# Optimization experiments

Hardware: AMD Instinct MI355X
Metric: run time of the kernel (lower is better)

The kernel has to match this reference:

```python
import jax, jax.numpy as jnp
import numpy as np

B, S, D, F, E = 4, 2048, 1024, 4096, 8


def setup_inputs() -> dict:
    key = jax.random.key(0)
    ks = jax.random.split(key, 7)
    s1 = 1.0 / np.sqrt(D)
    s2 = 1.0 / np.sqrt(F)
    x = jax.random.normal(ks[0], (B, S, D), dtype=jnp.float32)
    # Stacked expert weights: linear1 (D->F), linear2 (F->D), torch default uniform init
    W1 = jax.random.uniform(ks[1], (E, D, F), jnp.float32, -s1, s1)
    b1 = jax.random.uniform(ks[2], (E, F), jnp.float32, -s1, s1)
    W2 = jax.random.uniform(ks[3], (E, F, D), jnp.float32, -s2, s2)
    b2 = jax.random.uniform(ks[4], (E, D), jnp.float32, -s2, s2)
    Wr = jax.random.uniform(ks[5], (D, E), jnp.float32, -s1, s1)
    br = jax.random.uniform(ks[6], (E,), jnp.float32, -s1, s1)
    return {"x": x, "W1": W1, "b1": b1, "W2": W2, "b2": b2, "Wr": Wr, "br": br}


def reference(x, W1, b1, W2, b2, Wr, br):
    b, s, d = x.shape
    e = Wr.shape[1]
    logits = x @ Wr + br                      # [B,S,E]
    idx = jnp.argmax(logits, axis=-1)         # top-1 expert per token
    probs = jax.nn.softmax(logits, axis=-1)
    gates = jnp.take_along_axis(probs, idx[..., None], axis=-1)[..., 0]  # [B,S]
    xf = x.reshape(-1, d)                     # [N,D]
    idxf = idx.reshape(-1)
    gf = gates.reshape(-1)
    out = jnp.zeros_like(xf)
    for ei in range(e):                       # fixed small expert count
        h = jax.nn.gelu(xf @ W1[ei] + b1[ei], approximate=False)  # exact gelu like F.gelu
        y = h @ W2[ei] + b2[ei]
        mask = (idxf == ei).astype(xf.dtype)
        out = out + y * (gf * mask)[:, None]
    return out.reshape(b, s, d)
```

## Files before the change

### kernel.cpp

```cpp
#include <hip/hip_runtime.h>
#include <stdint.h>
#include <math.h>

#define NTOK 8192
#define DIM  1024
#define FDIM 4096
#define NEXP 8

typedef __bf16 bf16x8 __attribute__((ext_vector_type(8)));
typedef float floatx4 __attribute__((ext_vector_type(4)));
typedef unsigned int u32;

__device__ __forceinline__ unsigned short f2b(float f) {
  union { float f; unsigned u; } v; v.f = f;
  return (unsigned short)((v.u + 0x7fffu + ((v.u >> 16) & 1u)) >> 16);
}

__device__ __forceinline__ float gelu_f(float x) {
  float u = 1.5957691216f * x * (1.0f + 0.044715f * x * x);
  return x / (1.0f + __expf(-u));
}

__device__ __forceinline__ void async_cp16(const unsigned short* g, unsigned short* l) {
  __builtin_amdgcn_global_load_lds((__attribute__((address_space(1))) u32*)g,
                                   (__attribute__((address_space(3))) u32*)l, 16, 0, 0);
}

__device__ __forceinline__ void expert_tile(const int* __restrict__ ctrl, int mt,
                                            int& e, int& m0, int& cnt, int& ntiles) {
  int off = 0, ts = 0;
  e = 0; m0 = 0; cnt = 0;
#pragma unroll
  for (int i = 0; i < NEXP; i++) {
    int c = ctrl[i];
    int nt = (c + 127) >> 7;
    if (mt >= ts && mt < ts + nt) {
      e = i;
      m0 = off + (mt - ts) * 128;
      cnt = c - (mt - ts) * 128;
    }
    ts += nt; off += c;
  }
  ntiles = ts;
  if (cnt > 128) cnt = 128;
}

__global__ __launch_bounds__(256) void router_k(
    const float* __restrict__ x, const float* __restrict__ Wr,
    const float* __restrict__ br, int* __restrict__ idx,
    float* __restrict__ gate, int* __restrict__ ctrl) {
  int t = (int)((blockIdx.x * 256 + threadIdx.x) >> 6);
  int lane = threadIdx.x & 63;
  const float* xr = x + (size_t)t * DIM;
  float acc[NEXP];
#pragma unroll
  for (int e = 0; e < NEXP; e++) acc[e] = 0.f;
#pragma unroll
  for (int k = 0; k < DIM / 64; k++) {
    int d = k * 64 + lane;
    float xv = xr[d];
    const float4* wp = (const float4*)(Wr + (size_t)d * NEXP);
    float4 w0 = wp[0], w1 = wp[1];
    acc[0] += xv * w0.x; acc[1] += xv * w0.y;
    acc[2] += xv * w0.z; acc[3] += xv * w0.w;
    acc[4] += xv * w1.x; acc[5] += xv * w1.y;
    acc[6] += xv * w1.z; acc[7] += xv * w1.w;
  }
#pragma unroll
  for (int off = 32; off > 0; off >>= 1) {
#pragma unroll
    for (int e = 0; e < NEXP; e++) acc[e] += __shfl_xor(acc[e], off, 64);
  }
  if (lane == 0) {
    float mx = -3.4e38f; int best = 0;
#pragma unroll
    for (int e = 0; e < NEXP; e++) {
      float l = acc[e] + br[e];
      if (l > mx) { mx = l; best = e; }
    }
    float s = 0.f;
#pragma unroll
    for (int e = 0; e < NEXP; e++) s += expf(acc[e] + br[e] - mx);
    idx[t] = best;
    gate[t] = 1.f / s;
    atomicAdd(&ctrl[best], 1);
  }
}

__global__ __launch_bounds__(256) void scatter_k(
    const float* __restrict__ x, const int* __restrict__ idx,
    const float* __restrict__ gate, int* __restrict__ ctrl,
    unsigned short* __restrict__ Xb, int* __restrict__ token_dst,
    float* __restrict__ gate_p) {
  __shared__ int s_pos;
  int t = blockIdx.x;
  if (threadIdx.x == 0) {
    int e = idx[t];
    int off = 0;
#pragma unroll
    for (int i = 0; i < NEXP; i++) off += (i < e) ? ctrl[i] : 0;
    s_pos = off + atomicAdd(&ctrl[17 + e], 1);
  }
  __syncthreads();
  int pos = s_pos;
  if (threadIdx.x == 0) { token_dst[pos] = t; gate_p[pos] = gate[t]; }
  float4 v = ((const float4*)(x + (size_t)t * DIM))[threadIdx.x];
  ushort4 o;
  o.x = f2b(v.x); o.y = f2b(v.y); o.z = f2b(v.z); o.w = f2b(v.w);
  ((ushort4*)(Xb + (size_t)pos * DIM))[threadIdx.x] = o;
}

__global__ __launch_bounds__(256) void transpose_cvt2_k(
    const float* __restrict__ W1, unsigned short* __restrict__ W1b,
    const float* __restrict__ W2, unsigned short* __restrict__ W2b) {
  __shared__ float tile[64][65];
  __shared__ unsigned short obuf[64][72];
  int z = blockIdx.z;
  const float* in; unsigned short* out; int R, C, tc, tr;
  if (z < NEXP) {
    in = W1 + (size_t)z * DIM * FDIM; out = W1b + (size_t)z * DIM * FDIM;
    R = DIM; C = FDIM; tc = blockIdx.x; tr = blockIdx.y;
  } else {
    int e = z - NEXP;
    in = W2 + (size_t)e * FDIM * DIM; out = W2b + (size_t)e * FDIM * DIM;
    R = FDIM; C = DIM; tc = blockIdx.y; tr = blockIdx.x;
  }
  int c0 = tc * 64, r0 = tr * 64;
  int t = threadIdx.x;
  int rr = t >> 4, cc = (t & 15) * 4;
#pragma unroll
  for (int k = 0; k < 64; k += 16) {
    float4 v = *(const float4*)&in[(size_t)(r0 + rr + k) * C + c0 + cc];
    tile[rr + k][cc] = v.x; tile[rr + k][cc + 1] = v.y;
    tile[rr + k][cc + 2] = v.z; tile[rr + k][cc + 3] = v.w;
  }
  __syncthreads();
  int cr = t >> 4, rb = (t & 15) * 4;
#pragma unroll
  for (int k = 0; k < 64; k += 16) {
    ushort4 o;
    o.x = f2b(tile[rb + 0][cr + k]); o.y = f2b(tile[rb + 1][cr + k]);
    o.z = f2b(tile[rb + 2][cr + k]); o.w = f2b(tile[rb + 3][cr + k]);
    *(ushort4*)&obuf[cr + k][rb] = o;
  }
  __syncthreads();
  int r2 = t >> 3, c8 = (t & 7) * 8;
#pragma unroll
  for (int k = 0; k < 64; k += 32)
    *(uint4*)&out[(size_t)(c0 + r2 + k) * R + r0 + c8] = *(const uint4*)&obuf[r2 + k][c8];
}

__global__ __launch_bounds__(256) void gemm1_k(
    const unsigned short* __restrict__ Amat, const unsigned short* __restrict__ Bmat,
    const float* __restrict__ bias, unsigned short* __restrict__ Hout,
    const int* __restrict__ ctrl) {
  __shared__ unsigned short lds[17408];
  unsigned short* A_lds = lds;
  unsigned short* B_lds = lds + 8192;

  int mt = blockIdx.y;
  int e, m0, cnt, ntiles;
  expert_tile(ctrl, mt, e, m0, cnt, ntiles);
  if (mt >= ntiles) return;
  int c0 = blockIdx.x * 128;
  const unsigned short* B = Bmat + (size_t)e * FDIM * DIM;

  int tid = threadIdx.x;
  int lane = tid & 63, wave = tid >> 6;
  int wr = wave >> 1, wc = wave & 1;
  int grp = lane >> 4, m16 = lane & 15;

  int lr = lane >> 3;
  int cchunk = (lane & 7) ^ lr;
  const unsigned short* srcA[4];
  const unsigned short* srcB[4];
  unsigned short* dstA[4];
  unsigned short* dstB[4];
#pragma unroll
  for (int q = 0; q < 4; q++) {
    int brow = wave * 32 + q * 8;
    int arow = m0 + brow + lr; if (arow > NTOK - 1) arow = NTOK - 1;
    srcA[q] = Amat + (size_t)arow * DIM + cchunk * 8;
    srcB[q] = B + (size_t)(c0 + brow + lr) * DIM + cchunk * 8;
    dstA[q] = A_lds + brow * 64;
    dstB[q] = B_lds + brow * 64;
  }

  floatx4 acc[4][4];
  floatx4 zero = {0.f, 0.f, 0.f, 0.f};
#pragma unroll
  for (int i = 0; i < 4; i++)
#pragma unroll
    for (int j = 0; j < 4; j++) acc[i][j] = zero;

  int x7 = m16 & 7;
  int rowA[4], rowB[4];
#pragma unroll
  for (int i = 0; i < 4; i++) {
    rowA[i] = (wr * 64 + i * 16 + m16) * 64;
    rowB[i] = (wc * 64 + i * 16 + m16) * 64;
  }

  for (int kk = 0; kk < DIM; kk += 64) {
#pragma unroll
    for (int q = 0; q < 4; q++) async_cp16(srcA[q], dstA[q]);
#pragma unroll
    for (int q = 0; q < 4; q++) async_cp16(srcB[q], dstB[q]);
#pragma unroll
    for (int q = 0; q < 4; q++) { srcA[q] += 64; srcB[q] += 64; }
    __syncthreads();
    bf16x8 af[2][4], bfr[2][4];
#pragma unroll
    for (int h = 0; h < 2; h++) {
      int off = (((h << 2) | grp) ^ x7) << 3;
#pragma unroll
      for (int i = 0; i < 4; i++) {
        af[h][i]  = *(const bf16x8*)&A_lds[rowA[i] + off];
        bfr[h][i] = *(const bf16x8*)&B_lds[rowB[i] + off];
      }
    }
#pragma unroll
    for (int h = 0; h < 2; h++)
#pragma unroll
      for (int i = 0; i < 4; i++)
#pragma unroll
        for (int j = 0; j < 4; j++)
          acc[i][j] = __builtin_amdgcn_mfma_f32_16x16x32_bf16(af[h][i], bfr[h][j], acc[i][j], 0, 0, 0);
    __syncthreads();
  }

  float bs[4];
#pragma unroll
  for (int j = 0; j < 4; j++) bs[j] = bias[(size_t)e * FDIM + c0 + wc * 64 + j * 16 + m16];

  unsigned short* st = lds + wave * 4352;
#pragma unroll
  for (int i = 0; i < 4; i++)
#pragma unroll
    for (int j = 0; j < 4; j++)
#pragma unroll
      for (int r = 0; r < 4; r++)
        st[(i * 16 + grp * 4 + r) * 68 + j * 16 + m16] = f2b(gelu_f(acc[i][j][r] + bs[j]));
  __syncthreads();
  int lr8 = lane >> 3, c8 = (lane & 7) * 8;
  int colb = c0 + wc * 64 + c8;
#pragma unroll
  for (int rr = 0; rr < 8; rr++) {
    int row = rr * 8 + lr8;
    int gm = wr * 64 + row;
    if (gm < cnt) {
      uint2 a = *(const uint2*)&st[row * 68 + c8];
      uint2 b = *(const uint2*)&st[row * 68 + c8 + 4];
      uint4 v; v.x = a.x; v.y = a.y; v.z = b.x; v.w = b.y;
      *(uint4*)&Hout[(size_t)(m0 + gm) * FDIM + colb] = v;
    }
  }
}

__global__ __launch_bounds__(256) void gemm2_k(
    const unsigned short* __restrict__ Hmat, const unsigned short* __restrict__ W2b,
    const float* __restrict__ b2, float* __restrict__ out,
    const int* __restrict__ token_dst, const float* __restrict__ gate_p,
    const int* __restrict__ ctrl) {
  __shared__ unsigned short lds[32768];

  int mt = blockIdx.y;
  int e, m0, cnt, ntiles;
  expert_tile(ctrl, mt, e, m0, cnt, ntiles);
  if (mt >= ntiles) return;
  int c0 = blockIdx.x * 128;
  const unsigned short* B = W2b + (size_t)e * DIM * FDIM;

  int tid = threadIdx.x;
  int lane = tid & 63, wave = tid >> 6;
  int wr = wave >> 1, wc = wave & 1;
  int grp = lane >> 4, m16 = lane & 15;

  int lr = lane >> 3;
  int cchunk = (lane & 7) ^ lr;
  const unsigned short* srcA[4];
  const unsigned short* srcB[4];
  int dstoff[4];
#pragma unroll
  for (int q = 0; q < 4; q++) {
    int brow = wave * 32 + q * 8;
    int arow = m0 + brow + lr; if (arow > NTOK - 1) arow = NTOK - 1;
    srcA[q] = Hmat + (size_t)arow * FDIM + cchunk * 8;
    srcB[q] = B + (size_t)(c0 + brow + lr) * FDIM + cchunk * 8;
    dstoff[q] = brow * 64;
  }

  floatx4 acc[4][4];
  floatx4 zero = {0.f, 0.f, 0.f, 0.f};
#pragma unroll
  for (int i = 0; i < 4; i++)
#pragma unroll
    for (int j = 0; j < 4; j++) acc[i][j] = zero;

  int x7 = m16 & 7;
  int rowA[4], rowB[4];
#pragma unroll
  for (int i = 0; i < 4; i++) {
    rowA[i] = (wr * 64 + i * 16 + m16) * 64;
    rowB[i] = (wc * 64 + i * 16 + m16) * 64;
  }

#pragma unroll
  for (int q = 0; q < 4; q++) async_cp16(srcA[q], lds + dstoff[q]);
#pragma unroll
  for (int q = 0; q < 4; q++) async_cp16(srcB[q], lds + 8192 + dstoff[q]);
#pragma unroll
  for (int q = 0; q < 4; q++) { srcA[q] += 64; srcB[q] += 64; }

  const int kIters = FDIM / 64;
  int p = 0;
  for (int it = 0; it < kIters; ++it) {
    __syncthreads();
    unsigned short* Acur = lds + p * 16384;
    unsigned short* Bcur = Acur + 8192;
    if (it + 1 < kIters) {
      unsigned short* An = lds + (p ^ 1) * 16384;
      unsigned short* Bn = An + 8192;
#pragma unroll
      for (int q = 0; q < 4; q++) async_cp16(srcA[q], An + dstoff[q]);
#pragma unroll
      for (int q = 0; q < 4; q++) async_cp16(srcB[q], Bn + dstoff[q]);
#pragma unroll
      for (int q = 0; q < 4; q++) { srcA[q] += 64; srcB[q] += 64; }
    }
    bf16x8 af[2][4], bfr[2][4];
#pragma unroll
    for (int h = 0; h < 2; h++) {
      int off = (((h << 2) | grp) ^ x7) << 3;
#pragma unroll
      for (int i = 0; i < 4; i++) {
        af[h][i]  = *(const bf16x8*)&Acur[rowA[i] + off];
        bfr[h][i] = *(const bf16x8*)&Bcur[rowB[i] + off];
      }
    }
#pragma unroll
    for (int h = 0; h < 2; h++)
#pragma unroll
      for (int i = 0; i < 4; i++)
#pragma unroll
        for (int j = 0; j < 4; j++)
          acc[i][j] = __builtin_amdgcn_mfma_f32_16x16x32_bf16(af[h][i], bfr[h][j], acc[i][j], 0, 0, 0);
    p ^= 1;
  }

  float bs[4];
#pragma unroll
  for (int j = 0; j < 4; j++) bs[j] = b2[(size_t)e * DIM + c0 + wc * 64 + j * 16 + m16];

#pragma unroll
  for (int i = 0; i < 4; i++) {
    int rb = wr * 64 + i * 16 + grp * 4;
#pragma unroll
    for (int r = 0; r < 4; r++) {
      int lm = rb + r;
      if (lm < cnt) {
        int t = token_dst[m0 + lm];
        float g = gate_p[m0 + lm];
#pragma unroll
        for (int j = 0; j < 4; j++) {
          int col = c0 + wc * 64 + j * 16 + m16;
          out[(size_t)t * DIM + col] = (acc[i][j][r] + bs[j]) * g;
        }
      }
    }
  }
}

extern "C" void kernel_launch(void* const* d_in, const int* in_sizes, int n_in,
                              void* d_out, int out_size, void* d_ws, size_t ws_size,
                              hipStream_t stream) {
  const float* x  = (const float*)d_in[0];
  const float* W1 = (const float*)d_in[1];
  const float* b1 = (const float*)d_in[2];
  const float* W2 = (const float*)d_in[3];
  const float* b2 = (const float*)d_in[4];
  const float* Wr = (const float*)d_in[5];
  const float* br = (const float*)d_in[6];
  float* out = (float*)d_out;

  char* w = (char*)d_ws;
  int*   ctrl      = (int*)w;
  int*   idx       = (int*)(w + 1024);
  float* gate      = (float*)(w + 1024 + 4 * NTOK);
  int*   token_dst = (int*)(w + 1024 + 8 * NTOK);
  float* gate_p    = (float*)(w + 1024 + 12 * NTOK);
  unsigned short* Xb  = (unsigned short*)(w + (1ull << 18));
  unsigned short* H   = (unsigned short*)(w + (20ull << 20));
  unsigned short* W1b = (unsigned short*)(w + (88ull << 20));
  unsigned short* W2b = (unsigned short*)(w + (156ull << 20));

  hipMemsetAsync(ctrl, 0, 256, stream);
  router_k<<<NTOK / 4, 256, 0, stream>>>(x, Wr, br, idx, gate, ctrl);
  scatter_k<<<NTOK, 256, 0, stream>>>(x, idx, gate, ctrl, Xb, token_dst, gate_p);
  transpose_cvt2_k<<<dim3(64, 16, 16), 256, 0, stream>>>(W1, W1b, W2, W2b);
  gemm1_k<<<dim3(FDIM / 128, 72), 256, 0, stream>>>(Xb, W1b, b1, H, ctrl);
  gemm2_k<<<dim3(DIM / 128, 72), 256, 0, stream>>>(H, W2b, b2, out, token_dst, gate_p, ctrl);
}
```

Measured before the change: 781.2 us.

## Fuse bf16 conversion into router and gather tokens via permutation in gemm1

The router kernel now writes a bf16 copy of x in token order, and a small perm kernel builds only the expert-sorted permutation and gathered gates. This replaces the per-token scatter kernel that re-read x and wrote a sorted bf16 copy. gemm1 gathers A rows through the permutation indices, and its epilogue staging buffer switches from padded rows to an XOR-swizzled layout that uses less LDS. The aim is to remove one full pass over x and a launch of 8192 small blocks, at the cost of indirect, non-contiguous row loads in gemm1.

```diff
diff --git a/kernel.cpp b/kernel.cpp
--- a/kernel.cpp
+++ b/kernel.cpp
@@ -45,13 +45,15 @@
   if (cnt > 128) cnt = 128;
 }
 
-__global__ __launch_bounds__(256) void router_k(
+__global__ __launch_bounds__(256) void router_cvt_k(
     const float* __restrict__ x, const float* __restrict__ Wr,
     const float* __restrict__ br, int* __restrict__ idx,
-    float* __restrict__ gate, int* __restrict__ ctrl) {
+    float* __restrict__ gate, int* __restrict__ ctrl,
+    unsigned short* __restrict__ Xc) {
   int t = (int)((blockIdx.x * 256 + threadIdx.x) >> 6);
   int lane = threadIdx.x & 63;
   const float* xr = x + (size_t)t * DIM;
+  unsigned short* xo = Xc + (size_t)t * DIM;
   float acc[NEXP];
 #pragma unroll
   for (int e = 0; e < NEXP; e++) acc[e] = 0.f;
@@ -59,6 +61,7 @@
   for (int k = 0; k < DIM / 64; k++) {
     int d = k * 64 + lane;
     float xv = xr[d];
+    xo[d] = f2b(xv);
     const float4* wp = (const float4*)(Wr + (size_t)d * NEXP);
     float4 w0 = wp[0], w1 = wp[1];
     acc[0] += xv * w0.x; acc[1] += xv * w0.y;
@@ -87,27 +90,17 @@
   }
 }
 
-__global__ __launch_bounds__(256) void scatter_k(
-    const float* __restrict__ x, const int* __restrict__ idx,
-    const float* __restrict__ gate, int* __restrict__ ctrl,
-    unsigned short* __restrict__ Xb, int* __restrict__ token_dst,
-    float* __restrict__ gate_p) {
-  __shared__ int s_pos;
-  int t = blockIdx.x;
-  if (threadIdx.x == 0) {
-    int e = idx[t];
-    int off = 0;
-#pragma unroll
-    for (int i = 0; i < NEXP; i++) off += (i < e) ? ctrl[i] : 0;
-    s_pos = off + atomicAdd(&ctrl[17 + e], 1);
-  }
-  __syncthreads();
-  int pos = s_pos;
-  if (threadIdx.x == 0) { token_dst[pos] = t; gate_p[pos] = gate[t]; }
-  float4 v = ((const float4*)(x + (size_t)t * DIM))[threadIdx.x];
-  ushort4 o;
-  o.x = f2b(v.x); o.y = f2b(v.y); o.z = f2b(v.z); o.w = f2b(v.w);
-  ((ushort4*)(Xb + (size_t)pos * DIM))[threadIdx.x] = o;
+__global__ __launch_bounds__(256) void perm_k(
+    const int* __restrict__ idx, const float* __restrict__ gate,
+    int* __restrict__ ctrl, int* __restrict__ perm, float* __restrict__ gate_p) {
+  int t = blockIdx.x * 256 + threadIdx.x;
+  int e = idx[t];
+  int off = 0;
+#pragma unroll
+  for (int i = 0; i < NEXP; i++) off += (i < e) ? ctrl[i] : 0;
+  int pos = off + atomicAdd(&ctrl[17 + e], 1);
+  perm[pos] = t;
+  gate_p[pos] = gate[t];
 }
 
 __global__ __launch_bounds__(256) void transpose_cvt2_k(
@@ -151,10 +144,10 @@
 }
 
 __global__ __launch_bounds__(256) void gemm1_k(
-    const unsigned short* __restrict__ Amat, const unsigned short* __restrict__ Bmat,
+    const unsigned short* __restrict__ Xc, const unsigned short* __restrict__ Bmat,
     const float* __restrict__ bias, unsigned short* __restrict__ Hout,
-    const int* __restrict__ ctrl) {
-  __shared__ unsigned short lds[17408];
+    const int* __restrict__ ctrl, const int* __restrict__ perm) {
+  __shared__ unsigned short lds[16384];
   unsigned short* A_lds = lds;
   unsigned short* B_lds = lds + 8192;
 
@@ -179,8 +172,9 @@
 #pragma unroll
   for (int q = 0; q < 4; q++) {
     int brow = wave * 32 + q * 8;
-    int arow = m0 + brow + lr; if (arow > NTOK - 1) arow = NTOK - 1;
-    srcA[q] = Amat + (size_t)arow * DIM + cchunk * 8;
+    int p = m0 + brow + lr; if (p > NTOK - 1) p = NTOK - 1;
+    int arow = perm[p];
+    srcA[q] = Xc + (size_t)arow * DIM + cchunk * 8;
     srcB[q] = B + (size_t)(c0 + brow + lr) * DIM + cchunk * 8;
     dstA[q] = A_lds + brow * 64;
     dstB[q] = B_lds + brow * 64;
@@ -233,14 +227,17 @@
 #pragma unroll
   for (int j = 0; j < 4; j++) bs[j] = bias[(size_t)e * FDIM + c0 + wc * 64 + j * 16 + m16];
 
-  unsigned short* st = lds + wave * 4352;
+  unsigned short* st = lds + wave * 4096;
 #pragma unroll
   for (int i = 0; i < 4; i++)
 #pragma unroll
     for (int j = 0; j < 4; j++)
 #pragma unroll
-      for (int r = 0; r < 4; r++)
-        st[(i * 16 + grp * 4 + r) * 68 + j * 16 + m16] = f2b(gelu_f(acc[i][j][r] + bs[j]));
+      for (int r = 0; r < 4; r++) {
+        int row = i * 16 + grp * 4 + r;
+        int scol = (j * 16 + m16) ^ (((row >> 1) & 7) << 3);
+        st[row * 64 + scol] = f2b(gelu_f(acc[i][j][r] + bs[j]));
+      }
   __syncthreads();
   int lr8 = lane >> 3, c8 = (lane & 7) * 8;
   int colb = c0 + wc * 64 + c8;
@@ -249,10 +246,8 @@
     int row = rr * 8 + lr8;
     int gm = wr * 64 + row;
     if (gm < cnt) {
-      uint2 a = *(const uint2*)&st[row * 68 + c8];
-      uint2 b = *(const uint2*)&st[row * 68 + c8 + 4];
-      uint4 v; v.x = a.x; v.y = a.y; v.z = b.x; v.w = b.y;
-      *(uint4*)&Hout[(size_t)(m0 + gm) * FDIM + colb] = v;
+      int scol = c8 ^ (((row >> 1) & 7) << 3);
+      *(uint4*)&Hout[(size_t)(m0 + gm) * FDIM + colb] = *(const uint4*)&st[row * 64 + scol];
     }
   }
 }
@@ -260,7 +255,7 @@
 __global__ __launch_bounds__(256) void gemm2_k(
     const unsigned short* __restrict__ Hmat, const unsigned short* __restrict__ W2b,
     const float* __restrict__ b2, float* __restrict__ out,
-    const int* __restrict__ token_dst, const float* __restrict__ gate_p,
+    const int* __restrict__ perm, const float* __restrict__ gate_p,
     const int* __restrict__ ctrl) {
   __shared__ unsigned short lds[32768];
 
@@ -359,7 +354,7 @@
     for (int r = 0; r < 4; r++) {
       int lm = rb + r;
       if (lm < cnt) {
-        int t = token_dst[m0 + lm];
+        int t = perm[m0 + lm];
         float g = gate_p[m0 + lm];
 #pragma unroll
         for (int j = 0; j < 4; j++) {
@@ -384,20 +379,20 @@
   float* out = (float*)d_out;
 
   char* w = (char*)d_ws;
-  int*   ctrl      = (int*)w;
-  int*   idx       = (int*)(w + 1024);
-  float* gate      = (float*)(w + 1024 + 4 * NTOK);
-  int*   token_dst = (int*)(w + 1024 + 8 * NTOK);
-  float* gate_p    = (float*)(w + 1024 + 12 * NTOK);
-  unsigned short* Xb  = (unsigned short*)(w + (1ull << 18));
+  int*   ctrl   = (int*)w;
+  int*   idx    = (int*)(w + 1024);
+  float* gate   = (float*)(w + 1024 + 4 * NTOK);
+  int*   perm   = (int*)(w + 1024 + 8 * NTOK);
+  float* gate_p = (float*)(w + 1024 + 12 * NTOK);
+  unsigned short* Xc  = (unsigned short*)(w + (1ull << 18));
   unsigned short* H   = (unsigned short*)(w + (20ull << 20));
   unsigned short* W1b = (unsigned short*)(w + (88ull << 20));
   unsigned short* W2b = (unsigned short*)(w + (156ull << 20));
 
   hipMemsetAsync(ctrl, 0, 256, stream);
-  router_k<<<NTOK / 4, 256, 0, stream>>>(x, Wr, br, idx, gate, ctrl);
-  scatter_k<<<NTOK, 256, 0, stream>>>(x, idx, gate, ctrl, Xb, token_dst, gate_p);
   transpose_cvt2_k<<<dim3(64, 16, 16), 256, 0, stream>>>(W1, W1b, W2, W2b);
-  gemm1_k<<<dim3(FDIM / 128, 72), 256, 0, stream>>>(Xb, W1b, b1, H, ctrl);
-  gemm2_k<<<dim3(DIM / 128, 72), 256, 0, stream>>>(H, W2b, b2, out, token_dst, gate_p, ctrl);
-}
+  router_cvt_k<<<NTOK / 4, 256, 0, stream>>>(x, Wr, br, idx, gate, ctrl, Xc);
+  perm_k<<<NTOK / 256, 256, 0, stream>>>(idx, gate, ctrl, perm, gate_p);
+  gemm1_k<<<dim3(FDIM / 128, 72), 256, 0, stream>>>(Xc, W1b, b1, H, ctrl, perm);
+  gemm2_k<<<dim3(DIM / 128, 72), 256, 0, stream>>>(H, W2b, b2, out, perm, gate_p, ctrl);
+}
```

Result: faster. 714.8 us (-8.5%).
